# Optimization experiments

Measured on AMD Instinct MI355X. Metric: run time of the kernel, lower is better.

## Reference

```python
import jax, jax.numpy as jnp
import numpy as np

B, T, C, H, D = 2, 2048, 768, 12, 64
ATTN_MULT = 0.125  # 1/sqrt(head_dim)


def setup_inputs() -> dict:
    key = jax.random.key(0)
    k0, k1, k2 = jax.random.split(key, 3)
    x = jax.random.normal(k0, (B, T, C), jnp.float32)
    w_attn = jax.random.normal(k1, (3 * H * D, C), jnp.float32) * 0.02
    b_attn = jnp.zeros((3 * H * D,), jnp.float32)
    w_proj = jax.random.normal(k2, (C, H * D), jnp.float32) * 0.02
    b_proj = jnp.zeros((C,), jnp.float32)
    return {"x": x, "w_attn": w_attn, "b_attn": b_attn, "w_proj": w_proj, "b_proj": b_proj}


def reference(x, w_attn, b_attn, w_proj, b_proj):
    Bx, Tx, Cx = x.shape
    # fused qkv projection (torch nn.Linear: x @ W^T + b)
    qkv = x @ w_attn.T + b_attn                      # [B,T,3*H*D]
    q, k, v = jnp.split(qkv, 3, axis=2)
    def to_heads(t):
        return t.reshape(Bx, Tx, H, D).transpose(0, 2, 1, 3)  # [B,H,T,D]
    q, k, v = to_heads(q), to_heads(k), to_heads(v)
    att = jnp.einsum('bhqd,bhkd->bhqk', q, k) * ATTN_MULT     # [B,H,T,T]

    causal = jnp.tril(jnp.ones((Tx, Tx), dtype=bool))
    # selection scores from head 0 (selective attention)
    S = jax.nn.relu(att[:, 0])                                # [B,T,T]
    # prevent_from_masking_myself: zero diagonal; protect_bos_token: zero key col 0
    smask = causal & ~jnp.eye(Tx, dtype=bool)
    smask = smask.at[:, 0].set(False)
    S = jnp.where(smask, S, 0.0)
    # exclusive cumulative sum over the query dim: F[i,j] = sum_{i'<i} S[i',j]
    Fmask = jnp.cumsum(S, axis=-2) - S                        # [B,T,T]
    att = att - Fmask[:, None]                                # broadcast over heads

    att = jnp.where(causal, att, -jnp.inf)
    p = jax.nn.softmax(att, axis=-1)                          # [B,H,T,T]
    y = jnp.einsum('bhqk,bhkd->bhqd', p, v)                   # [B,H,T,D]
    y = y.transpose(0, 2, 1, 3).reshape(Bx, Tx, H * D)
    return y @ w_proj.T + b_proj
```

## Files before the change

kernel.cpp:

```cpp
#include <hip/hip_runtime.h>
#include <hip/hip_bf16.h>

#define BB 2
#define TT 2048
#define CC 768
#define HH 12
#define DD 64
#define NQKV 2304
#define MTOT (BB*TT)
#define CH 32
#define NCH (TT/CH)

typedef __bf16 bf16x8 __attribute__((ext_vector_type(8)));
typedef __bf16 bf16x4 __attribute__((ext_vector_type(4)));
typedef float  f32x4  __attribute__((ext_vector_type(4)));

__device__ __forceinline__ f32x4 mfma16(bf16x8 a, bf16x8 b, f32x4 c) {
    return __builtin_amdgcn_mfma_f32_16x16x32_bf16(a, b, c, 0, 0, 0);
}

__device__ __forceinline__ void load_lds16(const void* g, void* l) {
    __builtin_amdgcn_global_load_lds(
        (const __attribute__((address_space(1))) void*)g,
        (__attribute__((address_space(3))) void*)l, 16, 0, 0);
}

__global__ __launch_bounds__(256) void cvt_bf16_kernel(
    const float* __restrict__ x, const float* __restrict__ wa, const float* __restrict__ wp,
    __bf16* __restrict__ xb, __bf16* __restrict__ wab, __bf16* __restrict__ wpb)
{
    const long NX = (long)MTOT * CC;
    const long NWA = (long)NQKV * CC;
    long idx = ((long)blockIdx.x * 256 + threadIdx.x) * 4;
    const float* src; __bf16* dst; long off;
    if (idx < NX)            { src = x;  dst = xb;  off = idx; }
    else if (idx < NX + NWA) { src = wa; dst = wab; off = idx - NX; }
    else                     { src = wp; dst = wpb; off = idx - NX - NWA; }
    float4 v = *(const float4*)(src + off);
    bf16x4 o;
    o[0] = (__bf16)v.x; o[1] = (__bf16)v.y; o[2] = (__bf16)v.z; o[3] = (__bf16)v.w;
    *(bf16x4*)(dst + off) = o;
}

template<int EPI>
__global__ __launch_bounds__(256, 2) void gemm_nt_kernel(
    const __bf16* __restrict__ A, const __bf16* __restrict__ Bw,
    const float* __restrict__ bias,
    __bf16* __restrict__ oQ, __bf16* __restrict__ oK, __bf16* __restrict__ oVT,
    float* __restrict__ oOut, int K)
{
    __shared__ __align__(16) __bf16 As[128 * 32];
    __shared__ __align__(16) __bf16 Bs[128 * 32];
    const int tid = threadIdx.x;
    const int m0 = blockIdx.y * 128, n0 = blockIdx.x * 128;
    const int w = tid >> 6, lane = tid & 63, quad = lane >> 4, l16 = lane & 15;
    const int wm = (w >> 1) * 64, wn = (w & 1) * 64;
    const int grow = w * 16 + (lane >> 2);
    const int gcol = (lane & 3) * 8;
    __bf16* AsW = As + w * 512;
    __bf16* BsW = Bs + w * 512;

    f32x4 acc[4][4] = {};

    for (int kt = 0; kt < K; kt += 32) {
        __syncthreads();
        load_lds16(A  + (long)(m0 + grow) * K + kt + gcol,      AsW);
        load_lds16(A  + (long)(m0 + grow + 64) * K + kt + gcol, AsW + 2048);
        load_lds16(Bw + (long)(n0 + grow) * K + kt + gcol,      BsW);
        load_lds16(Bw + (long)(n0 + grow + 64) * K + kt + gcol, BsW + 2048);
        __syncthreads();

        bf16x8 af[4], bfr[4];
#pragma unroll
        for (int g = 0; g < 4; g++)  af[g]  = *(const bf16x8*)(As + (wm + g * 16 + l16) * 32 + quad * 8);
#pragma unroll
        for (int jb = 0; jb < 4; jb++) bfr[jb] = *(const bf16x8*)(Bs + (wn + jb * 16 + l16) * 32 + quad * 8);
#pragma unroll
        for (int g = 0; g < 4; g++)
#pragma unroll
            for (int jb = 0; jb < 4; jb++)
                acc[g][jb] = mfma16(af[g], bfr[jb], acc[g][jb]);
    }

#pragma unroll
    for (int jb = 0; jb < 4; jb++) {
        const int n = n0 + wn + jb * 16 + l16;
        const float bv = bias[n];
#pragma unroll
        for (int g = 0; g < 4; g++) {
#pragma unroll
            for (int r = 0; r < 4; r++) {
                const int m = m0 + wm + g * 16 + quad * 4 + r;
                const float v = acc[g][jb][r] + bv;
                if (EPI == 0) {
                    const int which = n / 768;
                    const int rem = n - which * 768;
                    const int h = rem >> 6, d = rem & 63;
                    const int b = m >> 11, t = m & 2047;
                    const __bf16 hv = (__bf16)v;
                    if (which == 0)      oQ [(((b * HH + h) * TT + t) << 6) + d] = hv;
                    else if (which == 1) oK [(((b * HH + h) * TT + t) << 6) + d] = hv;
                    else                 oVT[((((b * HH + h) << 6) + d) * TT) + t] = hv;
                } else {
                    oOut[(long)m * CC + n] = v;
                }
            }
        }
    }
}

__global__ __launch_bounds__(256) void sgemm_kernel(
    const __bf16* __restrict__ q, const __bf16* __restrict__ k, __bf16* __restrict__ S)
{
    const int tj = blockIdx.x, ti = blockIdx.y, b = blockIdx.z;
    if (tj > ti) return;
    const int w = threadIdx.x >> 6, lane = threadIdx.x & 63, quad = lane >> 4, l16 = lane & 15;
    const int i0 = ti * 64 + w * 16;

    const __bf16* qp = q + (((long)(b * HH + 0) * TT + i0 + l16) << 6) + quad * 8;
    bf16x8 a0 = *(const bf16x8*)qp, a1 = *(const bf16x8*)(qp + 32);
    const __bf16* kbase = k + ((long)(b * HH + 0) * TT << 6);

#pragma unroll
    for (int jb = 0; jb < 4; jb++) {
        const __bf16* kp = kbase + (((long)(tj * 64 + jb * 16 + l16)) << 6) + quad * 8;
        bf16x8 b0 = *(const bf16x8*)kp, b1 = *(const bf16x8*)(kp + 32);
        f32x4 acc = {};
        acc = mfma16(a0, b0, acc);
        acc = mfma16(a1, b1, acc);
        const int j = tj * 64 + jb * 16 + l16;
#pragma unroll
        for (int r = 0; r < 4; r++) {
            const int i = i0 + quad * 4 + r;
            float v = fmaxf(acc[r] * 0.125f, 0.0f);
            v = (j >= 1 && j < i) ? v : 0.0f;
            S[((long)b * TT + i) * TT + j] = (__bf16)v;
        }
    }
}

__global__ __launch_bounds__(256) void scan_sum_kernel(
    const __bf16* __restrict__ S, float* __restrict__ csum)
{
    const int j = blockIdx.x * 256 + threadIdx.x;
    const int chunk = blockIdx.y, b = blockIdx.z;
    const int ib = chunk * CH;
    const __bf16* p = S + ((long)b * TT + ib) * TT + j;
    float s = 0.0f;
#pragma unroll
    for (int ii = 0; ii < CH; ii++) {
        float v = (float)p[(long)ii * TT];
        s += ((ib + ii) > j) ? v : 0.0f;
    }
    csum[(b * NCH + chunk) * TT + j] = s;
}

__global__ __launch_bounds__(256) void scan_prefix_kernel(float* __restrict__ csum)
{
    const int idx = blockIdx.x * 256 + threadIdx.x;
    const int b = idx >> 11, j = idx & 2047;
    float vals[NCH];
#pragma unroll
    for (int c = 0; c < NCH; c++) vals[c] = csum[(b * NCH + c) * TT + j];
    float off = 0.0f;
#pragma unroll
    for (int c = 0; c < NCH; c++) { float t = vals[c]; vals[c] = off; off += t; }
#pragma unroll
    for (int c = 0; c < NCH; c++) csum[(b * NCH + c) * TT + j] = vals[c];
}

__global__ __launch_bounds__(256) void scan_write_kernel(
    const __bf16* __restrict__ S, const float* __restrict__ csum, __bf16* __restrict__ Fo)
{
    const int j = blockIdx.x * 256 + threadIdx.x;
    const int chunk = blockIdx.y, b = blockIdx.z;
    const int ib = chunk * CH;
    float off = csum[(b * NCH + chunk) * TT + j];
    const __bf16* ps = S  + ((long)b * TT + ib) * TT + j;
    __bf16*       pf = Fo + ((long)b * TT + ib) * TT + j;
#pragma unroll
    for (int ii = 0; ii < CH; ii++) {
        float v = ((ib + ii) > j) ? (float)ps[(long)ii * TT] : 0.0f;
        pf[(long)ii * TT] = (__bf16)off;
        off += v;
    }
}

__global__ __launch_bounds__(128, 2) void flash_kernel(
    const __bf16* __restrict__ q, const __bf16* __restrict__ k, const __bf16* __restrict__ vT,
    const __bf16* __restrict__ F, __bf16* __restrict__ y)
{
    __shared__ __align__(16) __bf16 Ks[2][64 * 64];
    __shared__ __align__(16) __bf16 Vs[2][64 * 64];
    __shared__ __align__(16) __bf16 Pls[2][16 * 72];
    const int bid = blockIdx.x, h = blockIdx.y, b = blockIdx.z;
    const int w = threadIdx.x >> 6, lane = threadIdx.x & 63, quad = lane >> 4, l16 = lane & 15;
    const int rl = lane >> 3;
    const int cs8 = ((lane & 7) ^ rl) * 8;
    const int sw0 = ((quad)     ^ (l16 & 7)) * 8;
    const int sw1 = ((quad + 4) ^ (l16 & 7)) * 8;
    __bf16* Pl = &Pls[w][0];
    const __bf16* kb = k  + ((long)(b * HH + h) * TT << 6);
    const __bf16* vb = vT + ((long)(b * HH + h) * TT << 6);
    const __bf16* Fbase = F + (long)b * TT * TT;

    const int qt0 = bid, qt1 = 63 - bid;
    const int n0 = (qt0 >> 1) + 1, n1 = (qt1 >> 1) + 1;
    const int N = n0 + n1;

    int i0 = qt0 * 32 + w * 16;
    const __bf16* qp = q + (((long)(b * HH + h) * TT + i0 + l16) << 6) + quad * 8;
    bf16x8 aq0 = *(const bf16x8*)qp;
    bf16x8 aq1 = *(const bf16x8*)(qp + 32);

    f32x4 O[4] = {};
    float lr[4] = {0.0f, 0.0f, 0.0f, 0.0f};
    __bf16 Fn[4][4];

    {
        __bf16* KsW = Ks[0] + w * 2048;
        __bf16* VsW = Vs[0] + w * 2048;
#pragma unroll
        for (int t = 0; t < 4; t++)
            load_lds16(kb + ((long)(w * 32 + t * 8 + rl) << 6) + cs8, KsW + t * 512);
#pragma unroll
        for (int t = 0; t < 4; t++)
            load_lds16(vb + (long)(w * 32 + t * 8 + rl) * TT + cs8, VsW + t * 512);
        const __bf16* Fb = Fbase + (long)i0 * TT;
#pragma unroll
        for (int jh = 0; jh < 4; jh++)
#pragma unroll
            for (int r = 0; r < 4; r++)
                Fn[jh][r] = Fb[(long)(quad * 4 + r) * TT + jh * 16 + l16];
    }

    for (int it = 0; it < N; it++) {
        const int ph = (it >= n0);
        const int jt = (it - (ph ? n0 : 0)) << 6;
        const int qt = ph ? qt1 : qt0;
        const int jtend = (qt >> 1) << 6;

        __syncthreads();

        __bf16 Fc[4][4];
#pragma unroll
        for (int jh = 0; jh < 4; jh++)
#pragma unroll
            for (int r = 0; r < 4; r++)
                Fc[jh][r] = Fn[jh][r];

        if (it + 1 < N) {
            const int ph2 = (it + 1 >= n0);
            const int jt2 = ((it + 1) - (ph2 ? n0 : 0)) << 6;
            __bf16* KsW = Ks[(it + 1) & 1] + w * 2048;
            __bf16* VsW = Vs[(it + 1) & 1] + w * 2048;
#pragma unroll
            for (int t = 0; t < 4; t++)
                load_lds16(kb + ((long)(jt2 + w * 32 + t * 8 + rl) << 6) + cs8, KsW + t * 512);
#pragma unroll
            for (int t = 0; t < 4; t++)
                load_lds16(vb + (long)(w * 32 + t * 8 + rl) * TT + jt2 + cs8, VsW + t * 512);
            const int i0n = (ph2 ? qt1 : qt0) * 32 + w * 16;
            const __bf16* Fb2 = Fbase + (long)i0n * TT;
#pragma unroll
            for (int jh = 0; jh < 4; jh++)
#pragma unroll
                for (int r = 0; r < 4; r++)
                    Fn[jh][r] = Fb2[(long)(quad * 4 + r) * TT + jt2 + jh * 16 + l16];
        }
        __builtin_amdgcn_sched_barrier(0);

        const __bf16* Kc = Ks[it & 1];
        const __bf16* Vc = Vs[it & 1];
        float sc[4][4];
#pragma unroll
        for (int jh = 0; jh < 4; jh++) {
            const int jr = jh * 16 + l16;
            const bf16x8 kc0 = *(const bf16x8*)(Kc + (jr << 6) + sw0);
            const bf16x8 kc1 = *(const bf16x8*)(Kc + (jr << 6) + sw1);
            f32x4 acc = {};
            acc = mfma16(aq0, kc0, acc);
            acc = mfma16(aq1, kc1, acc);
#pragma unroll
            for (int r = 0; r < 4; r++) sc[jh][r] = acc[r];
        }
        if (jt == jtend) {
#pragma unroll
            for (int jh = 0; jh < 4; jh++) {
                const int j = jt + jh * 16 + l16;
#pragma unroll
                for (int r = 0; r < 4; r++) {
                    const int i = i0 + quad * 4 + r;
                    float v = fmaf(sc[jh][r], 0.125f, -(float)Fc[jh][r]);
                    v = (j <= i) ? v : -35.0f;
                    const float p = __expf(v);
                    sc[jh][r] = p;
                    lr[r] += p;
                }
            }
        } else {
#pragma unroll
            for (int jh = 0; jh < 4; jh++) {
#pragma unroll
                for (int r = 0; r < 4; r++) {
                    float v = fmaf(sc[jh][r], 0.125f, -(float)Fc[jh][r]);
                    const float p = __expf(v);
                    sc[jh][r] = p;
                    lr[r] += p;
                }
            }
        }
#pragma unroll
        for (int r = 0; r < 4; r++) {
            const int il = quad * 4 + r;
#pragma unroll
            for (int jh = 0; jh < 4; jh++)
                Pl[il * 72 + jh * 16 + l16] = (__bf16)sc[jh][r];
        }
        const bf16x8 ap0 = *(const bf16x8*)(Pl + l16 * 72 + quad * 8);
        const bf16x8 ap1 = *(const bf16x8*)(Pl + l16 * 72 + 32 + quad * 8);
#pragma unroll
        for (int db = 0; db < 4; db++) {
            const bf16x8 vv0 = *(const bf16x8*)(Vc + ((db * 16 + l16) << 6) + sw0);
            const bf16x8 vv1 = *(const bf16x8*)(Vc + ((db * 16 + l16) << 6) + sw1);
            O[db] = mfma16(ap0, vv0, O[db]);
            O[db] = mfma16(ap1, vv1, O[db]);
        }
        if (jt == jtend) {
            float inv[4];
#pragma unroll
            for (int r = 0; r < 4; r++) {
                float s = lr[r];
#pragma unroll
                for (int off = 8; off >= 1; off >>= 1) s += __shfl_xor(s, off, 16);
                inv[r] = 1.0f / s;
            }
#pragma unroll
            for (int db = 0; db < 4; db++) {
#pragma unroll
                for (int r = 0; r < 4; r++) {
                    const int i = i0 + quad * 4 + r;
                    y[((long)(b * TT + i)) * (HH * DD) + h * 64 + db * 16 + l16] = (__bf16)(O[db][r] * inv[r]);
                }
            }
#pragma unroll
            for (int db = 0; db < 4; db++) { O[db][0] = 0.f; O[db][1] = 0.f; O[db][2] = 0.f; O[db][3] = 0.f; }
            lr[0] = lr[1] = lr[2] = lr[3] = 0.0f;
            if (!ph) {
                i0 = qt1 * 32 + w * 16;
                const __bf16* qp2 = q + (((long)(b * HH + h) * TT + i0 + l16) << 6) + quad * 8;
                aq0 = *(const bf16x8*)qp2;
                aq1 = *(const bf16x8*)(qp2 + 32);
            }
        }
    }
}

extern "C" void kernel_launch(void* const* d_in, const int* in_sizes, int n_in,
                              void* d_out, int out_size, void* d_ws, size_t ws_size,
                              hipStream_t stream)
{
    const float* x      = (const float*)d_in[0];
    const float* w_attn = (const float*)d_in[1];
    const float* b_attn = (const float*)d_in[2];
    const float* w_proj = (const float*)d_in[3];
    const float* b_proj = (const float*)d_in[4];
    float* out = (float*)d_out;

    char* ws = (char*)d_ws;
    __bf16* xb  = (__bf16*)ws; ws += (long)MTOT * CC * 2;
    __bf16* wab = (__bf16*)ws; ws += (long)NQKV * CC * 2;
    __bf16* wpb = (__bf16*)ws; ws += (long)CC * (HH*DD) * 2;
    __bf16* qb  = (__bf16*)ws; ws += (long)BB * HH * TT * DD * 2;
    __bf16* kb  = (__bf16*)ws; ws += (long)BB * HH * TT * DD * 2;
    __bf16* vtb = (__bf16*)ws; ws += (long)BB * HH * TT * DD * 2;
    __bf16* SF  = (__bf16*)ws; ws += (long)BB * TT * TT * 2;
    __bf16* Fo  = (__bf16*)ws; ws += (long)BB * TT * TT * 2;
    float*  cs  = (float*)ws;  ws += (long)BB * NCH * TT * 4;
    __bf16* yb  = (__bf16*)ws; ws += (long)MTOT * (HH*DD) * 2;

    cvt_bf16_kernel<<<5376, 256, 0, stream>>>(x, w_attn, w_proj, xb, wab, wpb);
    gemm_nt_kernel<0><<<dim3(NQKV / 128, MTOT / 128), 256, 0, stream>>>(
        xb, wab, b_attn, qb, kb, vtb, nullptr, CC);
    sgemm_kernel<<<dim3(TT / 64, TT / 64, BB), 256, 0, stream>>>(qb, kb, SF);
    scan_sum_kernel<<<dim3(TT / 256, NCH, BB), 256, 0, stream>>>(SF, cs);
    scan_prefix_kernel<<<16, 256, 0, stream>>>(cs);
    scan_write_kernel<<<dim3(TT / 256, NCH, BB), 256, 0, stream>>>(SF, cs, Fo);
    flash_kernel<<<dim3(32, HH, BB), 128, 0, stream>>>(qb, kb, vtb, Fo, yb);
    gemm_nt_kernel<1><<<dim3((HH*DD) / 128, MTOT / 128), 256, 0, stream>>>(
        yb, wpb, b_proj, nullptr, nullptr, nullptr, out, HH * DD);
}
```

Baseline: 224.9 us.

## Write QKV row-major, add separate V transpose kernel, drop prefix-scan kernel

The QKV GEMM epilogue now stores a plain row-major [M,2304] bf16 buffer instead of scattering into per-head Q/K and transposed V. A new LDS-tiled kernel produces V^T, and the attention and selection-score kernels read Q and K with a 2304-element stride. The separate chunk-prefix kernel is removed; each scan_write block instead sums the preceding chunk totals itself. This trades scattered GEMM stores and one launch for an extra kernel pass over V, strided Q/K reads, and redundant prefix summation.

```diff
diff --git a/kernel.cpp b/kernel.cpp
--- a/kernel.cpp
+++ b/kernel.cpp
@@ -46,8 +46,7 @@
 __global__ __launch_bounds__(256, 2) void gemm_nt_kernel(
     const __bf16* __restrict__ A, const __bf16* __restrict__ Bw,
     const float* __restrict__ bias,
-    __bf16* __restrict__ oQ, __bf16* __restrict__ oK, __bf16* __restrict__ oVT,
-    float* __restrict__ oOut, int K)
+    __bf16* __restrict__ oBF, float* __restrict__ oF32, int K)
 {
     __shared__ __align__(16) __bf16 As[128 * 32];
     __shared__ __align__(16) __bf16 Bs[128 * 32];
@@ -82,6 +81,7 @@
                 acc[g][jb] = mfma16(af[g], bfr[jb], acc[g][jb]);
     }
 
+    const int ldc = (EPI == 0) ? NQKV : CC;
 #pragma unroll
     for (int jb = 0; jb < 4; jb++) {
         const int n = n0 + wn + jb * 16 + l16;
@@ -92,38 +92,52 @@
             for (int r = 0; r < 4; r++) {
                 const int m = m0 + wm + g * 16 + quad * 4 + r;
                 const float v = acc[g][jb][r] + bv;
-                if (EPI == 0) {
-                    const int which = n / 768;
-                    const int rem = n - which * 768;
-                    const int h = rem >> 6, d = rem & 63;
-                    const int b = m >> 11, t = m & 2047;
-                    const __bf16 hv = (__bf16)v;
-                    if (which == 0)      oQ [(((b * HH + h) * TT + t) << 6) + d] = hv;
-                    else if (which == 1) oK [(((b * HH + h) * TT + t) << 6) + d] = hv;
-                    else                 oVT[((((b * HH + h) << 6) + d) * TT) + t] = hv;
-                } else {
-                    oOut[(long)m * CC + n] = v;
-                }
-            }
-        }
+                if (EPI == 0) oBF[(long)m * ldc + n] = (__bf16)v;
+                else          oF32[(long)m * ldc + n] = v;
+            }
+        }
+    }
+}
+
+__global__ __launch_bounds__(256) void transpose_v_kernel(
+    const __bf16* __restrict__ qkv, __bf16* __restrict__ vT)
+{
+    __shared__ __bf16 Tl[64][72];
+    const int tt = blockIdx.x, h = blockIdx.y, b = blockIdx.z;
+    const int tid = threadIdx.x;
+    const int r8 = tid >> 3, c8 = (tid & 7) * 8;
+    const __bf16* src = qkv + (long)(b * TT + tt * 64) * NQKV + 1536 + h * 64;
+#pragma unroll
+    for (int p = 0; p < 2; p++) {
+        const int row = p * 32 + r8;
+        bf16x8 v = *(const bf16x8*)(src + (long)row * NQKV + c8);
+#pragma unroll
+        for (int e = 0; e < 8; e++) Tl[c8 + e][row] = v[e];
+    }
+    __syncthreads();
+    __bf16* dst = vT + ((long)(b * HH + h) << 6) * TT + tt * 64;
+#pragma unroll
+    for (int p = 0; p < 2; p++) {
+        const int d = p * 32 + r8;
+        *(bf16x8*)(dst + (long)d * TT + c8) = *(const bf16x8*)(&Tl[d][c8]);
     }
 }
 
 __global__ __launch_bounds__(256) void sgemm_kernel(
-    const __bf16* __restrict__ q, const __bf16* __restrict__ k, __bf16* __restrict__ S)
+    const __bf16* __restrict__ qkv, __bf16* __restrict__ S)
 {
     const int tj = blockIdx.x, ti = blockIdx.y, b = blockIdx.z;
     if (tj > ti) return;
     const int w = threadIdx.x >> 6, lane = threadIdx.x & 63, quad = lane >> 4, l16 = lane & 15;
     const int i0 = ti * 64 + w * 16;
 
-    const __bf16* qp = q + (((long)(b * HH + 0) * TT + i0 + l16) << 6) + quad * 8;
+    const __bf16* qp = qkv + (long)(b * TT + i0 + l16) * NQKV + quad * 8;
     bf16x8 a0 = *(const bf16x8*)qp, a1 = *(const bf16x8*)(qp + 32);
-    const __bf16* kbase = k + ((long)(b * HH + 0) * TT << 6);
+    const __bf16* kbase = qkv + (long)(b * TT) * NQKV + 768;
 
 #pragma unroll
     for (int jb = 0; jb < 4; jb++) {
-        const __bf16* kp = kbase + (((long)(tj * 64 + jb * 16 + l16)) << 6) + quad * 8;
+        const __bf16* kp = kbase + (long)(tj * 64 + jb * 16 + l16) * NQKV + quad * 8;
         bf16x8 b0 = *(const bf16x8*)kp, b1 = *(const bf16x8*)(kp + 32);
         f32x4 acc = {};
         acc = mfma16(a0, b0, acc);
@@ -155,27 +169,14 @@
     csum[(b * NCH + chunk) * TT + j] = s;
 }
 
-__global__ __launch_bounds__(256) void scan_prefix_kernel(float* __restrict__ csum)
-{
-    const int idx = blockIdx.x * 256 + threadIdx.x;
-    const int b = idx >> 11, j = idx & 2047;
-    float vals[NCH];
-#pragma unroll
-    for (int c = 0; c < NCH; c++) vals[c] = csum[(b * NCH + c) * TT + j];
-    float off = 0.0f;
-#pragma unroll
-    for (int c = 0; c < NCH; c++) { float t = vals[c]; vals[c] = off; off += t; }
-#pragma unroll
-    for (int c = 0; c < NCH; c++) csum[(b * NCH + c) * TT + j] = vals[c];
-}
-
 __global__ __launch_bounds__(256) void scan_write_kernel(
     const __bf16* __restrict__ S, const float* __restrict__ csum, __bf16* __restrict__ Fo)
 {
     const int j = blockIdx.x * 256 + threadIdx.x;
     const int chunk = blockIdx.y, b = blockIdx.z;
     const int ib = chunk * CH;
-    float off = csum[(b * NCH + chunk) * TT + j];
+    float off = 0.0f;
+    for (int c = 0; c < chunk; c++) off += csum[(b * NCH + c) * TT + j];
     const __bf16* ps = S  + ((long)b * TT + ib) * TT + j;
     __bf16*       pf = Fo + ((long)b * TT + ib) * TT + j;
 #pragma unroll
@@ -187,7 +188,7 @@
 }
 
 __global__ __launch_bounds__(128, 2) void flash_kernel(
-    const __bf16* __restrict__ q, const __bf16* __restrict__ k, const __bf16* __restrict__ vT,
+    const __bf16* __restrict__ qkv, const __bf16* __restrict__ vT,
     const __bf16* __restrict__ F, __bf16* __restrict__ y)
 {
     __shared__ __align__(16) __bf16 Ks[2][64 * 64];
@@ -200,8 +201,8 @@
     const int sw0 = ((quad)     ^ (l16 & 7)) * 8;
     const int sw1 = ((quad + 4) ^ (l16 & 7)) * 8;
     __bf16* Pl = &Pls[w][0];
-    const __bf16* kb = k  + ((long)(b * HH + h) * TT << 6);
-    const __bf16* vb = vT + ((long)(b * HH + h) * TT << 6);
+    const __bf16* kb = qkv + (long)(b * TT) * NQKV + 768 + h * 64;
+    const __bf16* vb = vT + ((long)(b * HH + h) << 6) * TT;
     const __bf16* Fbase = F + (long)b * TT * TT;
 
     const int qt0 = bid, qt1 = 63 - bid;
@@ -209,7 +210,7 @@
     const int N = n0 + n1;
 
     int i0 = qt0 * 32 + w * 16;
-    const __bf16* qp = q + (((long)(b * HH + h) * TT + i0 + l16) << 6) + quad * 8;
+    const __bf16* qp = qkv + (long)(b * TT + i0 + l16) * NQKV + h * 64 + quad * 8;
     bf16x8 aq0 = *(const bf16x8*)qp;
     bf16x8 aq1 = *(const bf16x8*)(qp + 32);
 
@@ -222,7 +223,7 @@
         __bf16* VsW = Vs[0] + w * 2048;
 #pragma unroll
         for (int t = 0; t < 4; t++)
-            load_lds16(kb + ((long)(w * 32 + t * 8 + rl) << 6) + cs8, KsW + t * 512);
+            load_lds16(kb + (long)(w * 32 + t * 8 + rl) * NQKV + cs8, KsW + t * 512);
 #pragma unroll
         for (int t = 0; t < 4; t++)
             load_lds16(vb + (long)(w * 32 + t * 8 + rl) * TT + cs8, VsW + t * 512);
@@ -256,7 +257,7 @@
             __bf16* VsW = Vs[(it + 1) & 1] + w * 2048;
 #pragma unroll
             for (int t = 0; t < 4; t++)
-                load_lds16(kb + ((long)(jt2 + w * 32 + t * 8 + rl) << 6) + cs8, KsW + t * 512);
+                load_lds16(kb + (long)(jt2 + w * 32 + t * 8 + rl) * NQKV + cs8, KsW + t * 512);
 #pragma unroll
             for (int t = 0; t < 4; t++)
                 load_lds16(vb + (long)(w * 32 + t * 8 + rl) * TT + jt2 + cs8, VsW + t * 512);
@@ -348,7 +349,7 @@
             lr[0] = lr[1] = lr[2] = lr[3] = 0.0f;
             if (!ph) {
                 i0 = qt1 * 32 + w * 16;
-                const __bf16* qp2 = q + (((long)(b * HH + h) * TT + i0 + l16) << 6) + quad * 8;
+                const __bf16* qp2 = qkv + (long)(b * TT + i0 + l16) * NQKV + h * 64 + quad * 8;
                 aq0 = *(const bf16x8*)qp2;
                 aq1 = *(const bf16x8*)(qp2 + 32);
             }
@@ -368,25 +369,24 @@
     float* out = (float*)d_out;
 
     char* ws = (char*)d_ws;
-    __bf16* xb  = (__bf16*)ws; ws += (long)MTOT * CC * 2;
-    __bf16* wab = (__bf16*)ws; ws += (long)NQKV * CC * 2;
-    __bf16* wpb = (__bf16*)ws; ws += (long)CC * (HH*DD) * 2;
-    __bf16* qb  = (__bf16*)ws; ws += (long)BB * HH * TT * DD * 2;
-    __bf16* kb  = (__bf16*)ws; ws += (long)BB * HH * TT * DD * 2;
-    __bf16* vtb = (__bf16*)ws; ws += (long)BB * HH * TT * DD * 2;
-    __bf16* SF  = (__bf16*)ws; ws += (long)BB * TT * TT * 2;
-    __bf16* Fo  = (__bf16*)ws; ws += (long)BB * TT * TT * 2;
-    float*  cs  = (float*)ws;  ws += (long)BB * NCH * TT * 4;
-    __bf16* yb  = (__bf16*)ws; ws += (long)MTOT * (HH*DD) * 2;
+    __bf16* xb   = (__bf16*)ws; ws += (long)MTOT * CC * 2;
+    __bf16* wab  = (__bf16*)ws; ws += (long)NQKV * CC * 2;
+    __bf16* wpb  = (__bf16*)ws; ws += (long)CC * (HH*DD) * 2;
+    __bf16* qkvb = (__bf16*)ws; ws += (long)MTOT * NQKV * 2;
+    __bf16* vtb  = (__bf16*)ws; ws += (long)BB * HH * TT * DD * 2;
+    __bf16* SF   = (__bf16*)ws; ws += (long)BB * TT * TT * 2;
+    __bf16* Fo   = (__bf16*)ws; ws += (long)BB * TT * TT * 2;
+    float*  cs   = (float*)ws;  ws += (long)BB * NCH * TT * 4;
+    __bf16* yb   = (__bf16*)ws; ws += (long)MTOT * (HH*DD) * 2;
 
     cvt_bf16_kernel<<<5376, 256, 0, stream>>>(x, w_attn, w_proj, xb, wab, wpb);
     gemm_nt_kernel<0><<<dim3(NQKV / 128, MTOT / 128), 256, 0, stream>>>(
-        xb, wab, b_attn, qb, kb, vtb, nullptr, CC);
-    sgemm_kernel<<<dim3(TT / 64, TT / 64, BB), 256, 0, stream>>>(qb, kb, SF);
+        xb, wab, b_attn, qkvb, nullptr, CC);
+    transpose_v_kernel<<<dim3(TT / 64, HH, BB), 256, 0, stream>>>(qkvb, vtb);
+    sgemm_kernel<<<dim3(TT / 64, TT / 64, BB), 256, 0, stream>>>(qkvb, SF);
     scan_sum_kernel<<<dim3(TT / 256, NCH, BB), 256, 0, stream>>>(SF, cs);
-    scan_prefix_kernel<<<16, 256, 0, stream>>>(cs);
     scan_write_kernel<<<dim3(TT / 256, NCH, BB), 256, 0, stream>>>(SF, cs, Fo);
-    flash_kernel<<<dim3(32, HH, BB), 128, 0, stream>>>(qb, kb, vtb, Fo, yb);
-    gemm_nt_kernel<1><<<dim3((HH*DD) / 128, MTOT / 128), 256, 0, stream>>>(
-        yb, wpb, b_proj, nullptr, nullptr, nullptr, out, HH * DD);
-}
+    flash_kernel<<<dim3(32, HH, BB), 128, 0, stream>>>(qkvb, vtb, Fo, yb);
+    gemm_nt_kernel<1><<<dim3(CC / 128, MTOT / 128), 256, 0, stream>>>(
+        yb, wpb, b_proj, nullptr, out, HH * DD);
+}
```

New measurement: 228.1 us. No clear change (+1.4%).
